# Performance work log

Measured on AMD Instinct MI355X. Metric: run time of the kernel, lower is better.

Reference implementation:

```python
import jax, jax.numpy as jnp
import numpy as np

N_NODES = 100000
N_EDGES = 3200000
IN_DIM = 256
OUT_DIM = 64


def setup_inputs() -> dict:
    key = jax.random.key(0)
    ks = jax.random.split(key, 12)
    x = jax.random.normal(ks[0], (N_NODES, IN_DIM), dtype=jnp.float32)
    edge_index = jax.random.randint(ks[1], (2, N_EDGES), 0, N_NODES, dtype=jnp.int64)
    s = 1.0 / np.sqrt(IN_DIM)
    so = 1.0 / np.sqrt(OUT_DIM)
    return {
        "x": x,
        "edge_index": edge_index,
        "W_hp": jax.random.uniform(ks[2], (IN_DIM, OUT_DIM), jnp.float32, -s, s),
        "b_hp": jnp.zeros((OUT_DIM,), jnp.float32),
        "W_lp": jax.random.uniform(ks[3], (IN_DIM, OUT_DIM), jnp.float32, -s, s),
        "b_lp": jnp.zeros((OUT_DIM,), jnp.float32),
        "W_i": jax.random.uniform(ks[4], (IN_DIM, OUT_DIM), jnp.float32, -s, s),
        "b_i": jnp.zeros((OUT_DIM,), jnp.float32),
        "w_gh": jax.random.uniform(ks[5], (OUT_DIM, 1), jnp.float32, -so, so),
        "b_gh": jnp.zeros((1,), jnp.float32),
        "w_gl": jax.random.uniform(ks[6], (OUT_DIM, 1), jnp.float32, -so, so),
        "b_gl": jnp.zeros((1,), jnp.float32),
        "w_gi": jax.random.uniform(ks[7], (OUT_DIM, 1), jnp.float32, -so, so),
        "b_gi": jnp.zeros((1,), jnp.float32),
    }


def _gcn_agg(h, src, dst, deg_isqrt, deg_inv, n):
    # A_hat @ h with GCN symmetric normalization and self-loops.
    norm = deg_isqrt[src] * deg_isqrt[dst]                    # [E]
    agg = jax.ops.segment_sum(h[src] * norm[:, None], dst, num_segments=n)
    return agg + deg_inv[:, None] * h                         # self-loop term


def reference(x, edge_index, W_hp, b_hp, W_lp, b_lp, W_i, b_i,
              w_gh, b_gh, w_gl, b_gl, w_gi, b_gi):
    n = x.shape[0]
    src, dst = edge_index[0], edge_index[1]
    # degrees with self-loops (counted on destination, PyG gcn_norm style)
    deg = jax.ops.segment_sum(jnp.ones_like(dst, dtype=x.dtype), dst, num_segments=n) + 1.0
    deg_isqrt = jax.lax.rsqrt(deg)
    deg_inv = 1.0 / deg

    h_hp = x @ W_hp + b_hp
    H_hp = jax.nn.relu(h_hp - _gcn_agg(h_hp, src, dst, deg_isqrt, deg_inv, n))  # HP = (I - A_hat) xW
    h_lp = x @ W_lp + b_lp
    H_lp = jax.nn.relu(_gcn_agg(h_lp, src, dst, deg_isqrt, deg_inv, n))         # LP = A_hat xW
    H_i = jax.nn.relu(x @ W_i + b_i)                                             # I  = xW

    sig_h = H_hp @ w_gh + b_gh   # [N,1] per-row gates
    sig_l = H_lp @ w_gl + b_gl
    sig_i = H_i @ w_gi + b_gi

    out = sig_h * H_hp + sig_l * H_lp + sig_i * H_i
    return jax.nn.log_softmax(out, axis=1)
```

## Files before the change

kernel.cpp:

```cpp
#include <hip/hip_runtime.h>
#include <hip/hip_bf16.h>
#include <hip/hip_fp16.h>

#define N_NODES 100000
#define N_EDGES 3200000
#define IN_DIM  256
#define OUT_DIM 64
#define NBUK2   512
#define BRANGE  196
#define BINBLK  256
#define CHUNK   (N_EDGES / BINBLK)
#define HTOT    (NBUK2 * BINBLK)
#define CAP     12288
#define SCLS_RANGE 12500

typedef __attribute__((ext_vector_type(8))) short short8;
typedef __attribute__((ext_vector_type(4))) float float4v;
typedef __attribute__((ext_vector_type(2))) float floatx2;
typedef __attribute__((ext_vector_type(4))) unsigned int uint4v;

__device__ __forceinline__ unsigned int enc_fp8_sw(float v) {
    unsigned int u = __float_as_uint(v);
    unsigned int s = (u >> 24) & 0x80u;
    unsigned int mag = u & 0x7fffffffu;
    unsigned int q;
    if (mag >= 0x43e00000u) q = 0x7e;
    else if (mag < 0x3c800000u) {
        float av = __uint_as_float(mag);
        q = (unsigned int)(av * 512.0f + 0.5f);
    } else {
        unsigned int mr = mag + 0x00080000u;
        unsigned int e = (mr >> 23) - 127 + 7;
        unsigned int m = (mr >> 20) & 7;
        q = (e << 3) | m;
        if (q > 0x7e) q = 0x7e;
    }
    return s | q;
}
__device__ __forceinline__ float dec_fp8_sw(unsigned int b) {
    unsigned int s = (b & 0x80u) << 24;
    unsigned int e = (b >> 3) & 15u, m = b & 7u;
    float f = (e == 0) ? (float)m * 0.001953125f
                       : __uint_as_float(((e + 120u) << 23) | (m << 20));
    return __uint_as_float(__float_as_uint(f) | s);
}

__device__ __forceinline__ unsigned short pack_fp8x2(float lo, float hi) {
#if __has_builtin(__builtin_amdgcn_cvt_pk_fp8_f32)
    int p = __builtin_amdgcn_cvt_pk_fp8_f32(lo, hi, 0, false);
    return (unsigned short)((unsigned int)p & 0xffffu);
#else
    return (unsigned short)(enc_fp8_sw(lo) | (enc_fp8_sw(hi) << 8));
#endif
}
template<bool HI>
__device__ __forceinline__ floatx2 cvt2(unsigned int w) {
#if __has_builtin(__builtin_amdgcn_cvt_pk_f32_fp8)
    return __builtin_amdgcn_cvt_pk_f32_fp8((int)w, HI);
#else
    unsigned int g = HI ? (w >> 16) : (w & 0xffffu);
    floatx2 r; r[0] = dec_fp8_sw(g & 0xffu); r[1] = dec_fp8_sw((g >> 8) & 0xffu);
    return r;
#endif
}

__device__ __forceinline__ bool detect_is64(const void* ei) {
    int tid = threadIdx.x;
    const int* e32 = (const int*)ei;
    int found = 0;
    for (int w = 2 * tid + 1; w < 8192; w += 2 * blockDim.x)
        found |= (e32[w] != 0);
    return __syncthreads_or(found) == 0;
}

__global__ __launch_bounds__(256) void hist_kernel(
    const void* __restrict__ ei, int* __restrict__ hist) {
    __shared__ int lh[NBUK2];
    bool is64 = detect_is64(ei);
    int tid = threadIdx.x;
    for (int b = tid; b < NBUK2; b += 256) lh[b] = 0;
    __syncthreads();
    int e0 = blockIdx.x * CHUNK, e1 = e0 + CHUNK;
    for (int e = e0 + tid; e < e1; e += 256) {
        int d = is64 ? (int)((const long long*)ei)[N_EDGES + e]
                     : ((const int*)ei)[N_EDGES + e];
        atomicAdd(&lh[(unsigned)d / BRANGE], 1);
    }
    __syncthreads();
    for (int b = tid; b < NBUK2; b += 256) hist[b * BINBLK + blockIdx.x] = lh[b];
}

__global__ __launch_bounds__(256) void hscan1_kernel(const int* __restrict__ hist,
                                                     int* __restrict__ hb) {
    __shared__ int red[256];
    int tid = threadIdx.x;
    red[tid] = hist[blockIdx.x * 256 + tid];
    __syncthreads();
    #pragma unroll
    for (int off = 128; off > 0; off >>= 1) {
        if (tid < off) red[tid] += red[tid + off];
        __syncthreads();
    }
    if (tid == 0) hb[blockIdx.x] = red[0];
}

__global__ __launch_bounds__(512) void hscan2_prep_kernel(
    int* __restrict__ hb,
    const float* __restrict__ Whp, const float* __restrict__ bhp,
    const float* __restrict__ Wlp, const float* __restrict__ blp,
    const float* __restrict__ Wi,  const float* __restrict__ bi,
    __hip_bfloat16* __restrict__ Wtf, float* __restrict__ biasAll) {
    __shared__ int sh[512];
    int tid = threadIdx.x;
    if (blockIdx.x == 0) {
        int v = hb[tid];
        sh[tid] = v;
        __syncthreads();
        int val = v;
        #pragma unroll
        for (int off = 1; off < 512; off <<= 1) {
            int t = (tid >= off) ? sh[tid - off] : 0;
            __syncthreads();
            val += t;
            sh[tid] = val;
            __syncthreads();
        }
        hb[tid] = val - v;
    } else {
        int gid = (blockIdx.x - 1) * 512 + tid;
        int frag = gid >> 6, j = gid & 63;
        int kk = frag / 12, slot = frag - kk * 12;
        int cl = j >> 2, kh = j & 3;
        int col = slot * 16 + cl;
        const float* W = (col < 64) ? Whp : (col < 128) ? Wlp : Wi;
        int c2 = col & 63;
        int k0 = kk * 32 + kh * 8;
        unsigned short tmp[8];
        #pragma unroll
        for (int i = 0; i < 8; ++i) {
            __hip_bfloat16 bv = __float2bfloat16(W[(k0 + i) * 64 + c2]);
            tmp[i] = *(unsigned short*)&bv;
        }
        *(short8*)((unsigned short*)Wtf + (size_t)gid * 8) = *(short8*)tmp;
        if (gid < 192) {
            const float* b = (gid < 64) ? bhp : (gid < 128) ? blp : bi;
            biasAll[gid] = b[gid & 63];
        }
    }
}

__global__ __launch_bounds__(256) void hscan3_kernel(const int* __restrict__ hist,
                                                     const int* __restrict__ hb,
                                                     int* __restrict__ pos) {
    __shared__ int sh[256];
    int tid = threadIdx.x;
    int i = blockIdx.x * 256 + tid;
    int v = hist[i];
    sh[tid] = v;
    __syncthreads();
    int val = v;
    #pragma unroll
    for (int off = 1; off < 256; off <<= 1) {
        int t = (tid >= off) ? sh[tid - off] : 0;
        __syncthreads();
        val += t;
        sh[tid] = val;
        __syncthreads();
    }
    pos[i] = hb[blockIdx.x] + val - v;
    if (i == HTOT - 1) pos[HTOT] = N_EDGES;
}

__global__ __launch_bounds__(256) void bin_kernel(
    const void* __restrict__ ei,
    const int* __restrict__ pos, unsigned int* __restrict__ binned) {
    __shared__ int lcur[NBUK2];
    bool is64 = detect_is64(ei);
    int tid = threadIdx.x;
    for (int b = tid; b < NBUK2; b += 256) lcur[b] = pos[b * BINBLK + blockIdx.x];
    __syncthreads();
    int e0 = blockIdx.x * CHUNK, e1 = e0 + CHUNK;
    for (int e = e0 + tid; e < e1; e += 256) {
        int s, d;
        if (is64) {
            s = (int)((const long long*)ei)[e];
            d = (int)((const long long*)ei)[N_EDGES + e];
        } else {
            s = ((const int*)ei)[e];
            d = ((const int*)ei)[N_EDGES + e];
        }
        int b = (int)((unsigned)d / BRANGE);
        int lnode = d - b * BRANGE;
        int p = atomicAdd(&lcur[b], 1);
        binned[p] = (unsigned)s | ((unsigned)lnode << 24);
    }
}

__global__ __launch_bounds__(256) void fill_kernel(
    const unsigned int* __restrict__ binned, const int* __restrict__ pos,
    unsigned int* __restrict__ csr, int* __restrict__ offs,
    float* __restrict__ isq, float* __restrict__ dinv) {
    __shared__ int ldeg2[BRANGE * 8];
    __shared__ int lpre[256];
    __shared__ unsigned int stag[CAP];

    int b = blockIdx.x;
    int ns = b * BRANGE;
    if (ns >= N_NODES) return;
    int ne = ns + BRANGE; if (ne > N_NODES) ne = N_NODES;
    int nn = ne - ns;
    int nsb = nn * 8;
    int lo = pos[b * BINBLK];
    int hi = pos[(b + 1) * BINBLK];
    int nb = hi - lo;
    int tid = threadIdx.x;

    for (int i = tid; i < nsb; i += 256) ldeg2[i] = 0;
    __syncthreads();
    for (int e = lo + tid; e < hi; e += 256) {
        unsigned int r = binned[e];
        atomicAdd(&ldeg2[(r >> 24) * 8 + (r & 0xffffffu) / SCLS_RANGE], 1);
    }
    __syncthreads();

    int base = tid * 7;
    int loc[7];
    int s = 0;
    #pragma unroll
    for (int j = 0; j < 7; ++j) {
        int idx = base + j;
        int v = (idx < nsb) ? ldeg2[idx] : 0;
        loc[j] = s;
        s += v;
    }
    lpre[tid] = s;
    __syncthreads();
    int val = s;
    #pragma unroll
    for (int off = 1; off < 256; off <<= 1) {
        int t = (tid >= off) ? lpre[tid - off] : 0;
        __syncthreads();
        val += t;
        lpre[tid] = val;
        __syncthreads();
    }
    int ex0 = val - s;
    __syncthreads();
    #pragma unroll
    for (int j = 0; j < 7; ++j) {
        int idx = base + j;
        if (idx < nsb) ldeg2[idx] = ex0 + loc[j];
    }
    __syncthreads();

    if (tid < nn) {
        int p0 = ldeg2[tid * 8];
        int p1 = (tid == nn - 1) ? nb : ldeg2[tid * 8 + 8];
        int d = p1 - p0;
        offs[ns + tid] = lo + p0;
        float dr = (float)(d + 1);
        isq[ns + tid] = rsqrtf(dr);
        dinv[ns + tid] = 1.0f / dr;
    }
    if (tid == 0 && ne == N_NODES) offs[N_NODES] = hi;
    __syncthreads();

    if (nb <= CAP) {
        for (int e = lo + tid; e < hi; e += 256) {
            unsigned int r = binned[e];
            unsigned int src = r & 0xffffffu;
            int p = atomicAdd(&ldeg2[(r >> 24) * 8 + src / SCLS_RANGE], 1);
            stag[p] = src;
        }
        __syncthreads();
        for (int j = tid; j < nb; j += 256)
            csr[lo + j] = stag[j];
    } else {
        for (int e = lo + tid; e < hi; e += 256) {
            unsigned int r = binned[e];
            unsigned int src = r & 0xffffffu;
            int p = atomicAdd(&ldeg2[(r >> 24) * 8 + src / SCLS_RANGE], 1);
            csr[lo + p] = src;
        }
    }
}

__global__ __launch_bounds__(256, 4) void gemm_kernel(
    const float* __restrict__ x,
    const __hip_bfloat16* __restrict__ Wtf,
    const float* __restrict__ biasAll,
    const float* __restrict__ isq,
    unsigned short* __restrict__ hq,
    unsigned int* __restrict__ hg, unsigned short* __restrict__ hgi) {

    __shared__ __align__(16) unsigned char smem[33280];
    unsigned char* bchunk = smem + 8704;

    const int tid = threadIdx.x;
    const int node0 = blockIdx.x * 64;
    const int w = tid >> 6;
    const int lane = tid & 63;
    const int cl = lane & 15;
    const int kh = lane >> 4;

    float4v acc[12];
    #pragma unroll
    for (int s = 0; s < 12; ++s) acc[s] = (float4v){0.f, 0.f, 0.f, 0.f};

    int arr[4], acc_[4];
    #pragma unroll
    for (int j = 0; j < 4; ++j) {
        int f = j * 1024 + tid * 4;
        arr[j] = f >> 6; acc_[j] = f & 63;
    }

    float4v aR[4];
    #pragma unroll
    for (int j = 0; j < 4; ++j) {
        int node = node0 + arr[j];
        aR[j] = (node < N_NODES)
              ? *(const float4v*)(x + (size_t)node * 256 + 0 * 64 + acc_[j])
              : (float4v){0.f, 0.f, 0.f, 0.f};
    }

    #pragma unroll
    for (int c = 0; c < 4; ++c) {
        #pragma unroll
        for (int j = 0; j < 4; ++j) {
            __hip_bfloat16 b0 = __float2bfloat16(aR[j].x), b1 = __float2bfloat16(aR[j].y);
            __hip_bfloat16 b2 = __float2bfloat16(aR[j].z), b3 = __float2bfloat16(aR[j].w);
            unsigned int lo = (unsigned int)*(unsigned short*)&b0 | ((unsigned int)*(unsigned short*)&b1 << 16);
            unsigned int hi = (unsigned int)*(unsigned short*)&b2 | ((unsigned int)*(unsigned short*)&b3 << 16);
            *(uint2*)(smem + (size_t)arr[j] * 136 + (size_t)acc_[j] * 2) = make_uint2(lo, hi);
        }
        {
            const uint4v* bsrc = (const uint4v*)((const unsigned char*)Wtf + (size_t)c * 24576);
            uint4v* bdst = (uint4v*)bchunk;
            #pragma unroll
            for (int j = 0; j < 6; ++j)
                bdst[j * 256 + tid] = bsrc[j * 256 + tid];
        }
        __syncthreads();

        float4v aN[4];
        if (c < 3) {
            #pragma unroll
            for (int j = 0; j < 4; ++j) {
                int node = node0 + arr[j];
                aN[j] = (node < N_NODES)
                      ? *(const float4v*)(x + (size_t)node * 256 + (c + 1) * 64 + acc_[j])
                      : (float4v){0.f, 0.f, 0.f, 0.f};
            }
        }

        #pragma unroll
        for (int kkl = 0; kkl < 2; ++kkl) {
            short8 A = *(const short8*)(smem + (size_t)(16 * w + cl) * 136 + kkl * 64 + kh * 16);
            #pragma unroll
            for (int s = 0; s < 12; ++s) {
                short8 B = *(const short8*)(bchunk + (size_t)((kkl * 12 + s) * 64 + 4 * cl + kh) * 16);
                acc[s] = __builtin_amdgcn_mfma_f32_16x16x32_bf16(A, B, acc[s], 0, 0, 0);
            }
        }
        __syncthreads();
        if (c < 3) {
            #pragma unroll
            for (int j = 0; j < 4; ++j) aR[j] = aN[j];
        }
    }

    unsigned short* stq = (unsigned short*)smem;
    unsigned int*   sth = (unsigned int*)(smem + 8192);
    unsigned short* sti = (unsigned short*)(smem + 24576);

    float sqv[4];
    #pragma unroll
    for (int r = 0; r < 4; ++r) {
        int node = node0 + 16 * w + kh * 4 + r;
        sqv[r] = (node < N_NODES) ? isq[node] : 0.f;
    }
    #pragma unroll
    for (int g = 0; g < 4; ++g) {
        int d = g * 16 + cl;
        float bias_hp = biasAll[d];
        float bias_lp = biasAll[d + 64];
        float bias_i  = biasAll[d + 128];
        #pragma unroll
        for (int r = 0; r < 4; ++r) {
            int nl = 16 * w + kh * 4 + r;
            float vhp = acc[g][r] + bias_hp;
            float vlp = acc[g + 4][r] + bias_lp;
            float vi  = acc[g + 8][r] + bias_i;
            stq[nl * 64 + d] = pack_fp8x2(vhp * sqv[r], vlp * sqv[r]);
            __hip_bfloat16 bh = __float2bfloat16(vhp);
            __hip_bfloat16 bl = __float2bfloat16(vlp);
            __hip_bfloat16 bb = __float2bfloat16(vi);
            sth[nl * 64 + d] =
                (unsigned int)*(unsigned short*)&bh | ((unsigned int)*(unsigned short*)&bl << 16);
            sti[nl * 64 + d] = *(unsigned short*)&bb;
        }
    }
    __syncthreads();

    int nvalid = N_NODES - node0; if (nvalid > 64) nvalid = 64;
    uint2* hq2 = (uint2*)(hq + (size_t)node0 * 64);
    uint2* stq2 = (uint2*)stq;
    #pragma unroll
    for (int j = 0; j < 4; ++j) {
        int idx = j * 256 + tid;
        if ((idx >> 4) < nvalid) hq2[idx] = stq2[idx];
    }
    uint4v* hg4 = (uint4v*)(hg + (size_t)node0 * 64);
    uint4v* sth4 = (uint4v*)sth;
    #pragma unroll
    for (int j = 0; j < 4; ++j) {
        int idx = j * 256 + tid;
        if ((idx >> 4) < nvalid) hg4[idx] = sth4[idx];
    }
    uint2* hgi2 = (uint2*)(hgi + (size_t)node0 * 64);
    uint2* sti2 = (uint2*)sti;
    #pragma unroll
    for (int j = 0; j < 4; ++j) {
        int idx = j * 256 + tid;
        if ((idx >> 4) < nvalid) hgi2[idx] = sti2[idx];
    }
}

__device__ __forceinline__ float wave_sum(float x) {
    #pragma unroll
    for (int off = 32; off > 0; off >>= 1) x += __shfl_xor(x, off);
    return x;
}
__device__ __forceinline__ float wave_max(float x) {
    #pragma unroll
    for (int off = 32; off > 0; off >>= 1) x = fmaxf(x, __shfl_xor(x, off));
    return x;
}

__global__ __launch_bounds__(256) void agg_kernel(
    const unsigned short* __restrict__ hq,
    const unsigned int* __restrict__ hg,
    const unsigned short* __restrict__ hgi,
    const int* __restrict__ offs,
    const unsigned int* __restrict__ csr,
    const float* __restrict__ isq,
    const float* __restrict__ dinv,
    const float* __restrict__ w_gh, const float* __restrict__ b_gh,
    const float* __restrict__ w_gl, const float* __restrict__ b_gl,
    const float* __restrict__ w_gi, const float* __restrict__ b_gi,
    float* __restrict__ out) {
    __shared__ float xfh[4][520];
    __shared__ float xfl[4][520];

    int wid = threadIdx.x >> 6;
    int v = blockIdx.x * 4 + wid;
    int lane = threadIdx.x & 63;
    if (v >= N_NODES) return;

    int start = offs[v], end = offs[v + 1];

    unsigned int gv = hg[(size_t)v * 64 + lane];
    unsigned int gvi = (unsigned int)hgi[(size_t)v * 64 + lane];
    float isqv = isq[v];
    float dv = dinv[v];
    float wgh = w_gh[lane], wgl = w_gl[lane], wgi = w_gi[lane];

    const int slot = lane >> 3;
    const int oct  = lane & 7;
    const unsigned oct16 = (unsigned)oct * 16u;
    const char* hqB = (const char*)hq;

    floatx2 a2[8];
    #pragma unroll
    for (int j = 0; j < 8; ++j) a2[j] = (floatx2){0.f, 0.f};

    for (int j0 = start; j0 < end; j0 += 64) {
        int m = end - j0; if (m > 64) m = 64;
        unsigned int uu = 0;
        if (lane < m) uu = csr[j0 + lane];
        int mfull = m & ~7;
        for (int k0 = 0; k0 < mfull; k0 += 8) {
            unsigned int u = __shfl(uu, k0 + slot);
            uint4v g = *(const uint4v*)(hqB + (size_t)(u * 128u + oct16));
            a2[0] += cvt2<false>(g[0]); a2[1] += cvt2<true>(g[0]);
            a2[2] += cvt2<false>(g[1]); a2[3] += cvt2<true>(g[1]);
            a2[4] += cvt2<false>(g[2]); a2[5] += cvt2<true>(g[2]);
            a2[6] += cvt2<false>(g[3]); a2[7] += cvt2<true>(g[3]);
        }
        if (mfull < m) {
            int idx = mfull + slot;
            bool valid = idx < m;
            unsigned int u = __shfl(uu, valid ? idx : (m - 1));
            uint4v g = *(const uint4v*)(hqB + (size_t)(u * 128u + oct16));
            unsigned int zm = valid ? 0xffffffffu : 0u;
            #pragma unroll
            for (int dd = 0; dd < 4; ++dd) {
                unsigned int wv = g[dd] & zm;
                a2[2 * dd]     += cvt2<false>(wv);
                a2[2 * dd + 1] += cvt2<true>(wv);
            }
        }
    }

    #pragma unroll
    for (int j = 0; j < 8; ++j) {
        xfh[wid][slot * 65 + oct * 8 + j] = a2[j][0];
        xfl[wid][slot * 65 + oct * 8 + j] = a2[j][1];
    }
    float acc_hp = 0.f, acc_lp = 0.f;
    #pragma unroll
    for (int s = 0; s < 8; ++s) {
        acc_hp += xfh[wid][s * 65 + lane];
        acc_lp += xfl[wid][s * 65 + lane];
    }

    float agg_hp = acc_hp * isqv;
    float agg_lp = acc_lp * isqv;

    float hhp = __uint_as_float(gv << 16);
    float hlp = __uint_as_float(gv & 0xffff0000u);
    float hi  = __uint_as_float(gvi << 16);

    float Hhp = fmaxf(hhp - (agg_hp + dv * hhp), 0.f);
    float Hlp = fmaxf(agg_lp + dv * hlp, 0.f);
    float Hi  = fmaxf(hi, 0.f);

    __half2 p2 = __floats2half2_rn(Hhp * wgh, Hlp * wgl);
    #pragma unroll
    for (int off = 32; off > 0; off >>= 1) {
        int o = __shfl_xor(*(int*)&p2, off);
        p2 = __hadd2(p2, *(__half2*)&o);
    }
    float sh = __low2float(p2) + b_gh[0];
    float sl = __high2float(p2) + b_gl[0];
    float si = wave_sum(Hi * wgi) + b_gi[0];

    float o = sh * Hhp + sl * Hlp + si * Hi;
    float mx = wave_max(o);
    float se = wave_sum(expf(o - mx));
    out[(size_t)v * 64 + lane] = o - mx - logf(se);
}

static inline size_t align256(size_t v) { return (v + 255) & ~(size_t)255; }

extern "C" void kernel_launch(void* const* d_in, const int* in_sizes, int n_in,
                              void* d_out, int out_size, void* d_ws, size_t ws_size,
                              hipStream_t stream) {
    const float* x    = (const float*)d_in[0];
    const void*  ei   = d_in[1];
    const float* Whp  = (const float*)d_in[2];
    const float* bhp  = (const float*)d_in[3];
    const float* Wlp  = (const float*)d_in[4];
    const float* blp  = (const float*)d_in[5];
    const float* Wi   = (const float*)d_in[6];
    const float* bi   = (const float*)d_in[7];
    const float* w_gh = (const float*)d_in[8];
    const float* b_gh = (const float*)d_in[9];
    const float* w_gl = (const float*)d_in[10];
    const float* b_gl = (const float*)d_in[11];
    const float* w_gi = (const float*)d_in[12];
    const float* b_gi = (const float*)d_in[13];
    float* out = (float*)d_out;

    const int N = N_NODES, E = N_EDGES;

    char* base = (char*)d_ws;
    size_t off = 0;
    int* offs = (int*)(base + off);            off = align256(off + (size_t)(N + 1) * 4);
    float* isq = (float*)(base + off);         off = align256(off + (size_t)N * 4);
    float* dinv = (float*)(base + off);        off = align256(off + (size_t)N * 4);
    int* hist = (int*)(base + off);            off = align256(off + (size_t)HTOT * 4);
    int* hb = (int*)(base + off);              off = align256(off + 512 * 4);
    int* pos = (int*)(base + off);             off = align256(off + (size_t)(HTOT + 1) * 4);
    unsigned int* binned = (unsigned int*)(base + off); off = align256(off + (size_t)E * 4);
    unsigned int* csr = (unsigned int*)(base + off); off = align256(off + (size_t)E * 4);
    float* biasAll = (float*)(base + off);     off = align256(off + 192 * 4);
    __hip_bfloat16* Wtf = (__hip_bfloat16*)(base + off); off = align256(off + 96 * 64 * 16);
    unsigned short* hq = (unsigned short*)(base + off); off = align256(off + (size_t)N * 64 * 2);
    unsigned int* hg = (unsigned int*)(base + off);   off = align256(off + (size_t)N * 64 * 4);
    unsigned short* hgi = (unsigned short*)(base + off); off = align256(off + (size_t)N * 64 * 2);

    hist_kernel<<<BINBLK, 256, 0, stream>>>(ei, hist);
    hscan1_kernel<<<HTOT / 256, 256, 0, stream>>>(hist, hb);
    hscan2_prep_kernel<<<13, 512, 0, stream>>>(hb, Whp, bhp, Wlp, blp, Wi, bi, Wtf, biasAll);
    hscan3_kernel<<<HTOT / 256, 256, 0, stream>>>(hist, hb, pos);
    bin_kernel<<<BINBLK, 256, 0, stream>>>(ei, pos, binned);
    fill_kernel<<<NBUK2, 256, 0, stream>>>(binned, pos, csr, offs, isq, dinv);
    gemm_kernel<<<(N + 63) / 64, 256, 0, stream>>>(x, Wtf, biasAll, isq, hq, hg, hgi);
    agg_kernel<<<(N + 3) / 4, 256, 0, stream>>>(hq, hg, hgi, offs, csr, isq, dinv,
                                                w_gh, b_gh, w_gl, b_gl, w_gi, b_gi, out);
}
```

Before: 176.1 us.

## Load GEMM operands directly from global into MFMA registers, dropping LDS staging

```diff
diff --git a/kernel.cpp b/kernel.cpp
--- a/kernel.cpp
+++ b/kernel.cpp
@@ -293,8 +293,7 @@
     unsigned short* __restrict__ hq,
     unsigned int* __restrict__ hg, unsigned short* __restrict__ hgi) {
 
-    __shared__ __align__(16) unsigned char smem[33280];
-    unsigned char* bchunk = smem + 8704;
+    __shared__ __align__(16) unsigned char smem[32768];
 
     const int tid = threadIdx.x;
     const int node0 = blockIdx.x * 64;
@@ -303,69 +302,35 @@
     const int cl = lane & 15;
     const int kh = lane >> 4;
 
+    const int row = node0 + 16 * w + cl;
+    const bool valid = row < N_NODES;
+    const float* xrow = x + (size_t)row * 256 + kh * 8;
+    const unsigned short* bbase = (const unsigned short*)Wtf + (size_t)(4 * cl + kh) * 8;
+
     float4v acc[12];
     #pragma unroll
     for (int s = 0; s < 12; ++s) acc[s] = (float4v){0.f, 0.f, 0.f, 0.f};
 
-    int arr[4], acc_[4];
-    #pragma unroll
-    for (int j = 0; j < 4; ++j) {
-        int f = j * 1024 + tid * 4;
-        arr[j] = f >> 6; acc_[j] = f & 63;
-    }
-
-    float4v aR[4];
-    #pragma unroll
-    for (int j = 0; j < 4; ++j) {
-        int node = node0 + arr[j];
-        aR[j] = (node < N_NODES)
-              ? *(const float4v*)(x + (size_t)node * 256 + 0 * 64 + acc_[j])
-              : (float4v){0.f, 0.f, 0.f, 0.f};
-    }
-
-    #pragma unroll
-    for (int c = 0; c < 4; ++c) {
+    #pragma unroll
+    for (int kk = 0; kk < 8; ++kk) {
+        float4v a0 = {0.f, 0.f, 0.f, 0.f}, a1 = {0.f, 0.f, 0.f, 0.f};
+        if (valid) {
+            a0 = *(const float4v*)(xrow + kk * 32);
+            a1 = *(const float4v*)(xrow + kk * 32 + 4);
+        }
+        unsigned short t[8];
         #pragma unroll
-        for (int j = 0; j < 4; ++j) {
-            __hip_bfloat16 b0 = __float2bfloat16(aR[j].x), b1 = __float2bfloat16(aR[j].y);
-            __hip_bfloat16 b2 = __float2bfloat16(aR[j].z), b3 = __float2bfloat16(aR[j].w);
-            unsigned int lo = (unsigned int)*(unsigned short*)&b0 | ((unsigned int)*(unsigned short*)&b1 << 16);
-            unsigned int hi = (unsigned int)*(unsigned short*)&b2 | ((unsigned int)*(unsigned short*)&b3 << 16);
-            *(uint2*)(smem + (size_t)arr[j] * 136 + (size_t)acc_[j] * 2) = make_uint2(lo, hi);
-        }
-        {
-            const uint4v* bsrc = (const uint4v*)((const unsigned char*)Wtf + (size_t)c * 24576);
-            uint4v* bdst = (uint4v*)bchunk;
-            #pragma unroll
-            for (int j = 0; j < 6; ++j)
-                bdst[j * 256 + tid] = bsrc[j * 256 + tid];
-        }
-        __syncthreads();
-
-        float4v aN[4];
-        if (c < 3) {
-            #pragma unroll
-            for (int j = 0; j < 4; ++j) {
-                int node = node0 + arr[j];
-                aN[j] = (node < N_NODES)
-                      ? *(const float4v*)(x + (size_t)node * 256 + (c + 1) * 64 + acc_[j])
-                      : (float4v){0.f, 0.f, 0.f, 0.f};
-            }
-        }
-
+        for (int i = 0; i < 4; ++i) {
+            __hip_bfloat16 b0 = __float2bfloat16(a0[i]);
+            __hip_bfloat16 b1 = __float2bfloat16(a1[i]);
+            t[i] = *(unsigned short*)&b0;
+            t[i + 4] = *(unsigned short*)&b1;
+        }
+        short8 A = *(short8*)t;
         #pragma unroll
-        for (int kkl = 0; kkl < 2; ++kkl) {
-            short8 A = *(const short8*)(smem + (size_t)(16 * w + cl) * 136 + kkl * 64 + kh * 16);
-            #pragma unroll
-            for (int s = 0; s < 12; ++s) {
-                short8 B = *(const short8*)(bchunk + (size_t)((kkl * 12 + s) * 64 + 4 * cl + kh) * 16);
-                acc[s] = __builtin_amdgcn_mfma_f32_16x16x32_bf16(A, B, acc[s], 0, 0, 0);
-            }
-        }
-        __syncthreads();
-        if (c < 3) {
-            #pragma unroll
-            for (int j = 0; j < 4; ++j) aR[j] = aN[j];
+        for (int s = 0; s < 12; ++s) {
+            short8 B = *(const short8*)(bbase + (size_t)(kk * 12 + s) * 512);
+            acc[s] = __builtin_amdgcn_mfma_f32_16x16x32_bf16(A, B, acc[s], 0, 0, 0);
         }
     }
 
```

After: 200.4 us. 1.14x slower.
